# Performance work log

Hardware: AMD Instinct MI355X
Metric: run time of the kernel (lower is better)

## Reference

```python
import jax, jax.numpy as jnp
import numpy as np

WIDTH_POW = 10
WIDTH = 2 ** WIDTH_POW          # 1024
HALF = WIDTH // 2               # 512
DEPTH = 8                       # number of butterfly layers
BDEPTH = 10                     # steps per butterfly (= log2(width))
BATCH = 65536
NUM_IN = WIDTH
NUM_OUT = WIDTH


def setup_inputs() -> dict:
    key = jax.random.key(0)
    k1, k2, k3, k4, k5 = jax.random.split(key, 5)
    X = jax.random.normal(k1, (BATCH, NUM_IN), dtype=jnp.float32)
    # rotation angles uniform in [0, 2*pi): (depth, half_width, bdepth)
    bparams = jax.random.uniform(k2, (DEPTH, HALF, BDEPTH), dtype=jnp.float32) * (2.0 * np.pi)
    eps = 1.0 / WIDTH
    n_act = DEPTH - 1
    bias = jax.random.uniform(k3, (n_act, WIDTH), dtype=jnp.float32) * (2 * eps) - eps
    slope = jax.random.uniform(k4, (n_act, WIDTH), dtype=jnp.float32) * (2 * eps) - eps + 1.0
    scale = jax.random.uniform(k5, (n_act, WIDTH), dtype=jnp.float32) * (2 * eps) - eps + 1.0
    return {"X": X, "bparams": bparams, "bias": bias, "slope": slope, "scale": scale}


def _butterfly(X, params):
    """params: (half, bdepth). One OrthogonalButterfly layer."""
    def step(X, theta):
        c = jnp.cos(theta)          # (half,)
        s = jnp.sin(theta)
        X0 = X[:, :HALF]
        X1 = X[:, HALF:]
        n0 = X0 * c + X1 * s
        n1 = -X0 * s + X1 * c
        # perm: even i -> n0[i//2], odd i -> n1[i//2]  == interleave n0, n1
        Xn = jnp.stack([n0, n1], axis=-1).reshape(X.shape[0], WIDTH)
        return Xn, None
    X, _ = jax.lax.scan(step, X, params.T)  # iterate over bdepth
    return X


def _quintic(X, bias, slope, scale):
    u = jnp.clip((X * slope - bias) / scale, -1.0, 1.0)
    u2 = u * u
    return scale * (u * (1.875 + u2 * (-1.25 + 0.375 * u2)))


def reference(X, bparams, bias, slope, scale):
    # num_inputs == width, so the zero-padding concat is a no-op.
    for i in range(DEPTH):
        X = _butterfly(X, bparams[i])
        if i != DEPTH - 1:
            X = _quintic(X, bias[i], slope[i], scale[i])
    return X[:, :NUM_OUT]
```

## Files before the change

kernel.cpp:

```cpp
#include <hip/hip_runtime.h>
#include <hip/hip_bf16.h>

#define WIDTH   1024
#define HALF_W  512
#define DEPTH   8
#define BDEPTH  10
#define BATCH   65536
#define ROWS    16
#define S_R     32
#define S_H     520

typedef _Float16 v8h __attribute__((ext_vector_type(8)));
typedef float    v4f __attribute__((ext_vector_type(4)));

static __device__ __forceinline__ unsigned short f2h(float x) {
    _Float16 h = (_Float16)x;
    return __builtin_bit_cast(unsigned short, h);
}

__global__ void gen_mats(const float* __restrict__ bp, unsigned short* __restrict__ mats)
{
    const int bid = blockIdx.x;
    const int grp = bid & 31;
    const int ph  = (bid >> 5) & 1;
    const int L   = bid >> 6;
    const int tid = threadIdx.x;

    __shared__ float M[2][32][32];

    for (int i = tid; i < 1024; i += 64)
        M[0][i >> 5][i & 31] = ((i >> 5) == (i & 31)) ? 1.0f : 0.0f;
    __syncthreads();

    int buf = 0;
    for (int s = 0; s < 5; ++s) {
        const int t = ph * 5 + s;
        const int stride = 1 << (4 - s);
        for (int idx = tid; idx < 512; idx += 64) {
            const int a  = idx >> 5;
            const int c  = idx & 31;
            const int lo = ((a & ~(stride - 1)) << 1) | (a & (stride - 1));
            const int hi = lo | stride;
            const int p_low = (ph == 0) ? ((lo << 5) | grp) : ((grp << 5) | lo);
            const int j = (((p_low << t) | (p_low >> (10 - t))) & 1023) & 511;
            const float theta = bp[L * (HALF_W * BDEPTH) + j * BDEPTH + t];
            float sn, cs;
            sincosf(theta, &sn, &cs);
            const float xl = M[buf][lo][c];
            const float xh = M[buf][hi][c];
            M[1 - buf][lo][c] =  cs * xl + sn * xh;
            M[1 - buf][hi][c] = -sn * xl + cs * xh;
        }
        buf = 1 - buf;
        __syncthreads();
    }

    unsigned short* out = mats + (size_t)bid * 1024;
    for (int i = tid; i < 1024; i += 64) {
        const int nt   = i >> 9;
        const int lane = (i >> 3) & 63;
        const int jj   = i & 7;
        const int n = nt * 16 + (lane & 15);
        const int k = (lane >> 4) * 8 + jj;
        out[i] = f2h(M[buf][n][k]);
    }
}

__global__ void __launch_bounds__(256, 2) butterfly_net(
    const float* __restrict__ X,
    const unsigned short* __restrict__ mats,
    const float* __restrict__ bias,
    const float* __restrict__ slope,
    const float* __restrict__ scale,
    float* __restrict__ out)
{
    __shared__ unsigned short X1[32 * S_H];
    __shared__ unsigned short X2[32 * S_H];

    const int tid  = threadIdx.x;
    const int lane = tid & 63;
    const int w    = tid >> 6;
    const int lw   = lane & 15;
    const int q    = lane >> 4;
    const int row0 = blockIdx.x * ROWS;

    for (int it = 0; it < 16; ++it) {
        const int f = (it * 256 + tid) * 4;
        const int r = f >> 10;
        const int c = f & 1023;
        const float4 v = *(const float4*)(X + (size_t)(row0 + r) * WIDTH + c);
        const int h  = c >> 5;
        const int g0 = c & 31;
        X1[(g0 + 0) * S_H + r * S_R + h] = f2h(v.x);
        X1[(g0 + 1) * S_H + r * S_R + h] = f2h(v.y);
        X1[(g0 + 2) * S_H + r * S_R + h] = f2h(v.z);
        X1[(g0 + 3) * S_H + r * S_R + h] = f2h(v.w);
    }
    __syncthreads();

    for (int L = 0; L < DEPTH; ++L) {
        const unsigned short* m1 = mats + (size_t)(L * 2 + 0) * 32 * 1024;
        for (int s = 0; s < 2; ++s) {
            const int gbase = w * 8 + s * 4;
            v4f C[4][2];
            #pragma unroll
            for (int gi = 0; gi < 4; ++gi) {
                const int g = gbase + gi;
                const v8h A = *(const v8h*)&X1[g * S_H + lw * S_R + q * 8];
                #pragma unroll
                for (int nt = 0; nt < 2; ++nt) {
                    const v8h B = *(const v8h*)&m1[(size_t)g * 1024 + nt * 512 + lane * 8];
                    C[gi][nt] = __builtin_amdgcn_mfma_f32_16x16x32_f16(
                        A, B, (v4f){0.0f, 0.0f, 0.0f, 0.0f}, 0, 0, 0);
                }
            }
            #pragma unroll
            for (int nt = 0; nt < 2; ++nt) {
                const int hout = nt * 16 + lw;
                #pragma unroll
                for (int r = 0; r < 4; ++r) {
                    const int row = q * 4 + r;
                    ushort4 pk;
                    pk.x = f2h(C[0][nt][r]);
                    pk.y = f2h(C[1][nt][r]);
                    pk.z = f2h(C[2][nt][r]);
                    pk.w = f2h(C[3][nt][r]);
                    *(ushort4*)&X2[hout * S_H + row * S_R + gbase] = pk;
                }
            }
        }
        __syncthreads();

        const unsigned short* m2 = mats + (size_t)(L * 2 + 1) * 32 * 1024;
        const bool last = (L == DEPTH - 1);
        for (int s = 0; s < 2; ++s) {
            const int hbase = w * 8 + s * 4;
            v4f C[4][2];
            #pragma unroll
            for (int hi2 = 0; hi2 < 4; ++hi2) {
                const int h = hbase + hi2;
                const v8h A = *(const v8h*)&X2[h * S_H + lw * S_R + q * 8];
                #pragma unroll
                for (int nt = 0; nt < 2; ++nt) {
                    const v8h B = *(const v8h*)&m2[(size_t)h * 1024 + nt * 512 + lane * 8];
                    C[hi2][nt] = __builtin_amdgcn_mfma_f32_16x16x32_f16(
                        A, B, (v4f){0.0f, 0.0f, 0.0f, 0.0f}, 0, 0, 0);
                }
            }
            if (!last) {
                #pragma unroll
                for (int nt = 0; nt < 2; ++nt) {
                    const int gout = nt * 16 + lw;
                    float bia[4], slo[4], sca[4], rsc[4];
                    #pragma unroll
                    for (int hi2 = 0; hi2 < 4; ++hi2) {
                        const int p = (hbase + hi2) * 32 + gout;
                        bia[hi2] = bias [L * WIDTH + p];
                        slo[hi2] = slope[L * WIDTH + p];
                        sca[hi2] = scale[L * WIDTH + p];
                        rsc[hi2] = 1.0f / sca[hi2];
                    }
                    #pragma unroll
                    for (int r = 0; r < 4; ++r) {
                        const int row = q * 4 + r;
                        ushort4 pk;
                        unsigned short* pp = (unsigned short*)&pk;
                        #pragma unroll
                        for (int hi2 = 0; hi2 < 4; ++hi2) {
                            const float x = C[hi2][nt][r];
                            float u = (x * slo[hi2] - bia[hi2]) * rsc[hi2];
                            u = fminf(1.0f, fmaxf(-1.0f, u));
                            const float u2 = u * u;
                            const float y = sca[hi2] *
                                (u * (1.875f + u2 * (-1.25f + 0.375f * u2)));
                            pp[hi2] = f2h(y);
                        }
                        *(ushort4*)&X1[gout * S_H + row * S_R + hbase] = pk;
                    }
                }
            } else {
                #pragma unroll
                for (int nt = 0; nt < 2; ++nt) {
                    const int gout = nt * 16 + lw;
                    #pragma unroll
                    for (int hi2 = 0; hi2 < 4; ++hi2) {
                        const int h = hbase + hi2;
                        #pragma unroll
                        for (int r = 0; r < 4; ++r) {
                            const int row = q * 4 + r;
                            out[(size_t)(row0 + row) * WIDTH + h * 32 + gout] =
                                C[hi2][nt][r];
                        }
                    }
                }
            }
        }
        __syncthreads();
    }
}

extern "C" void kernel_launch(void* const* d_in, const int* in_sizes, int n_in,
                              void* d_out, int out_size, void* d_ws, size_t ws_size,
                              hipStream_t stream)
{
    const float* X     = (const float*)d_in[0];
    const float* bp    = (const float*)d_in[1];
    const float* bias  = (const float*)d_in[2];
    const float* slope = (const float*)d_in[3];
    const float* scale = (const float*)d_in[4];
    unsigned short* mats = (unsigned short*)d_ws;

    hipLaunchKernelGGL(gen_mats, dim3(512), dim3(64), 0, stream, bp, mats);
    hipLaunchKernelGGL(butterfly_net, dim3(BATCH / ROWS), dim3(256), 0, stream,
                       X, mats, bias, slope, scale, (float*)d_out);
}
```

Before: 708.4 us.

## Use single in-place swizzled LDS buffer, 32-row blocks, and precomputed activation params

Replaces the two padded LDS buffers with one XOR-swizzled 64KB buffer. A-fragments are loaded into registers and a barrier is taken before the results are written back in place. Blocks grow to 512 threads handling 32 rows, so each loaded B matrix fragment is reused across two row groups. A small pre-kernel folds bias, slope and scale into packed float4 coefficients, removing divides and separate loads from the activation. The input load is restructured to do strided reads per thread. The main risks are an extra barrier per stage and lower occupancy from the larger block and LDS footprint.

Result: slower. 1.110 ms (+56.6%).

```diff
diff --git a/kernel.cpp b/kernel.cpp
--- a/kernel.cpp
+++ b/kernel.cpp
@@ -1,21 +1,24 @@
 #include <hip/hip_runtime.h>
-#include <hip/hip_bf16.h>
 
 #define WIDTH   1024
 #define HALF_W  512
 #define DEPTH   8
 #define BDEPTH  10
 #define BATCH   65536
-#define ROWS    16
-#define S_R     32
-#define S_H     520
+#define ROWS    32
 
 typedef _Float16 v8h __attribute__((ext_vector_type(8)));
+typedef _Float16 v4h __attribute__((ext_vector_type(4)));
 typedef float    v4f __attribute__((ext_vector_type(4)));
 
 static __device__ __forceinline__ unsigned short f2h(float x) {
     _Float16 h = (_Float16)x;
     return __builtin_bit_cast(unsigned short, h);
+}
+
+static __device__ __forceinline__ int xoff(int slice, int r, int k) {
+    int b = (slice << 11) + (r << 6) + (k << 1);
+    return b ^ ((((r >> 1) ^ slice) & 7) << 4);
 }
 
 __global__ void gen_mats(const float* __restrict__ bp, unsigned short* __restrict__ mats)
@@ -66,136 +69,143 @@
     }
 }
 
-__global__ void __launch_bounds__(256, 2) butterfly_net(
+__global__ void fuse_act(const float* __restrict__ bias,
+                         const float* __restrict__ slope,
+                         const float* __restrict__ scale,
+                         float4* __restrict__ actT)
+{
+    const int i = blockIdx.x * 256 + threadIdx.x;
+    if (i < (DEPTH - 1) * WIDTH) {
+        const float b = bias[i], s = slope[i], c = scale[i];
+        const float r = 1.0f / c;
+        actT[i] = make_float4(s * r, b * r, c, 0.0f);
+    }
+}
+
+__global__ void __launch_bounds__(512, 4) butterfly_net(
     const float* __restrict__ X,
     const unsigned short* __restrict__ mats,
-    const float* __restrict__ bias,
-    const float* __restrict__ slope,
-    const float* __restrict__ scale,
+    const float4* __restrict__ actT,
     float* __restrict__ out)
 {
-    __shared__ unsigned short X1[32 * S_H];
-    __shared__ unsigned short X2[32 * S_H];
+    __shared__ unsigned char Xb[32 * 2048];
 
     const int tid  = threadIdx.x;
     const int lane = tid & 63;
-    const int w    = tid >> 6;
+    const int wv   = tid >> 6;
+    const int oct  = wv & 3;
+    const int rg   = wv >> 2;
     const int lw   = lane & 15;
     const int q    = lane >> 4;
     const int row0 = blockIdx.x * ROWS;
-
-    for (int it = 0; it < 16; ++it) {
-        const int f = (it * 256 + tid) * 4;
-        const int r = f >> 10;
-        const int c = f & 1023;
-        const float4 v = *(const float4*)(X + (size_t)(row0 + r) * WIDTH + c);
-        const int h  = c >> 5;
-        const int g0 = c & 31;
-        X1[(g0 + 0) * S_H + r * S_R + h] = f2h(v.x);
-        X1[(g0 + 1) * S_H + r * S_R + h] = f2h(v.y);
-        X1[(g0 + 2) * S_H + r * S_R + h] = f2h(v.z);
-        X1[(g0 + 3) * S_H + r * S_R + h] = f2h(v.w);
+    const int rbase = rg * 16;
+
+    {
+        const int g = tid & 31;
+        const int m = tid >> 5;
+        #pragma unroll
+        for (int it = 0; it < 8; ++it) {
+            const int cmb = it * 16 + m;
+            const int r   = cmb >> 2;
+            const int h0  = (cmb & 3) * 8;
+            const float* src = X + (size_t)(row0 + r) * WIDTH + (size_t)h0 * 32 + g;
+            v8h pk;
+            #pragma unroll
+            for (int j = 0; j < 8; ++j)
+                pk[j] = (_Float16)src[j * 32];
+            *(v8h*)(Xb + xoff(g, r, h0)) = pk;
+        }
     }
     __syncthreads();
 
     for (int L = 0; L < DEPTH; ++L) {
-        const unsigned short* m1 = mats + (size_t)(L * 2 + 0) * 32 * 1024;
-        for (int s = 0; s < 2; ++s) {
-            const int gbase = w * 8 + s * 4;
-            v4f C[4][2];
-            #pragma unroll
-            for (int gi = 0; gi < 4; ++gi) {
-                const int g = gbase + gi;
-                const v8h A = *(const v8h*)&X1[g * S_H + lw * S_R + q * 8];
+        const bool last = (L == DEPTH - 1);
+
+        {
+            const unsigned short* m1 = mats + (size_t)(L * 2 + 0) * 32 * 1024;
+            v8h aF[8];
+            #pragma unroll
+            for (int i = 0; i < 8; ++i)
+                aF[i] = *(const v8h*)(Xb + xoff(oct * 8 + i, rbase + lw, q * 8));
+            __syncthreads();
+            #pragma unroll
+            for (int s = 0; s < 2; ++s) {
+                const int gbase = oct * 8 + s * 4;
                 #pragma unroll
                 for (int nt = 0; nt < 2; ++nt) {
-                    const v8h B = *(const v8h*)&m1[(size_t)g * 1024 + nt * 512 + lane * 8];
-                    C[gi][nt] = __builtin_amdgcn_mfma_f32_16x16x32_f16(
-                        A, B, (v4f){0.0f, 0.0f, 0.0f, 0.0f}, 0, 0, 0);
+                    v4f C[4];
+                    #pragma unroll
+                    for (int gi = 0; gi < 4; ++gi) {
+                        const v8h B = *(const v8h*)&m1[(size_t)(gbase + gi) * 1024
+                                                       + nt * 512 + lane * 8];
+                        C[gi] = __builtin_amdgcn_mfma_f32_16x16x32_f16(
+                            aF[s * 4 + gi], B, (v4f){0.f, 0.f, 0.f, 0.f}, 0, 0, 0);
+                    }
+                    const int hout = nt * 16 + lw;
+                    #pragma unroll
+                    for (int r = 0; r < 4; ++r) {
+                        v4h pk = { (_Float16)C[0][r], (_Float16)C[1][r],
+                                   (_Float16)C[2][r], (_Float16)C[3][r] };
+                        *(v4h*)(Xb + xoff(hout, rbase + q * 4 + r, gbase)) = pk;
+                    }
                 }
             }
-            #pragma unroll
-            for (int nt = 0; nt < 2; ++nt) {
-                const int hout = nt * 16 + lw;
+            __syncthreads();
+        }
+
+        {
+            const unsigned short* m2 = mats + (size_t)(L * 2 + 1) * 32 * 1024;
+            v8h aF[8];
+            #pragma unroll
+            for (int i = 0; i < 8; ++i)
+                aF[i] = *(const v8h*)(Xb + xoff(oct * 8 + i, rbase + lw, q * 8));
+            __syncthreads();
+            #pragma unroll
+            for (int s = 0; s < 2; ++s) {
+                const int hbase = oct * 8 + s * 4;
                 #pragma unroll
-                for (int r = 0; r < 4; ++r) {
-                    const int row = q * 4 + r;
-                    ushort4 pk;
-                    pk.x = f2h(C[0][nt][r]);
-                    pk.y = f2h(C[1][nt][r]);
-                    pk.z = f2h(C[2][nt][r]);
-                    pk.w = f2h(C[3][nt][r]);
-                    *(ushort4*)&X2[hout * S_H + row * S_R + gbase] = pk;
+                for (int nt = 0; nt < 2; ++nt) {
+                    v4f C[4];
+                    #pragma unroll
+                    for (int hi = 0; hi < 4; ++hi) {
+                        const v8h B = *(const v8h*)&m2[(size_t)(hbase + hi) * 1024
+                                                       + nt * 512 + lane * 8];
+                        C[hi] = __builtin_amdgcn_mfma_f32_16x16x32_f16(
+                            aF[s * 4 + hi], B, (v4f){0.f, 0.f, 0.f, 0.f}, 0, 0, 0);
+                    }
+                    const int gout = nt * 16 + lw;
+                    if (!last) {
+                        float4 ac[4];
+                        #pragma unroll
+                        for (int hi = 0; hi < 4; ++hi)
+                            ac[hi] = actT[(size_t)L * WIDTH + (hbase + hi) * 32 + gout];
+                        #pragma unroll
+                        for (int r = 0; r < 4; ++r) {
+                            v4h pk;
+                            #pragma unroll
+                            for (int hi = 0; hi < 4; ++hi) {
+                                float u = fmaf(C[hi][r], ac[hi].x, -ac[hi].y);
+                                u = fminf(1.0f, fmaxf(-1.0f, u));
+                                const float u2 = u * u;
+                                const float p5 = fmaf(u2, 0.375f, -1.25f);
+                                const float p3 = fmaf(u2, p5, 1.875f);
+                                pk[hi] = (_Float16)(u * p3 * ac[hi].z);
+                            }
+                            *(v4h*)(Xb + xoff(gout, rbase + q * 4 + r, hbase)) = pk;
+                        }
+                    } else {
+                        #pragma unroll
+                        for (int hi = 0; hi < 4; ++hi) {
+                            #pragma unroll
+                            for (int r = 0; r < 4; ++r)
+                                out[(size_t)(row0 + rbase + q * 4 + r) * WIDTH
+                                    + (hbase + hi) * 32 + gout] = C[hi][r];
+                        }
+                    }
                 }
             }
-        }
-        __syncthreads();
-
-        const unsigned short* m2 = mats + (size_t)(L * 2 + 1) * 32 * 1024;
-        const bool last = (L == DEPTH - 1);
-        for (int s = 0; s < 2; ++s) {
-            const int hbase = w * 8 + s * 4;
-            v4f C[4][2];
-            #pragma unroll
-            for (int hi2 = 0; hi2 < 4; ++hi2) {
-                const int h = hbase + hi2;
-                const v8h A = *(const v8h*)&X2[h * S_H + lw * S_R + q * 8];
-                #pragma unroll
-                for (int nt = 0; nt < 2; ++nt) {
-                    const v8h B = *(const v8h*)&m2[(size_t)h * 1024 + nt * 512 + lane * 8];
-                    C[hi2][nt] = __builtin_amdgcn_mfma_f32_16x16x32_f16(
-                        A, B, (v4f){0.0f, 0.0f, 0.0f, 0.0f}, 0, 0, 0);
-                }
-            }
-            if (!last) {
-                #pragma unroll
-                for (int nt = 0; nt < 2; ++nt) {
-                    const int gout = nt * 16 + lw;
-                    float bia[4], slo[4], sca[4], rsc[4];
-                    #pragma unroll
-                    for (int hi2 = 0; hi2 < 4; ++hi2) {
-                        const int p = (hbase + hi2) * 32 + gout;
-                        bia[hi2] = bias [L * WIDTH + p];
-                        slo[hi2] = slope[L * WIDTH + p];
-                        sca[hi2] = scale[L * WIDTH + p];
-                        rsc[hi2] = 1.0f / sca[hi2];
-                    }
-                    #pragma unroll
-                    for (int r = 0; r < 4; ++r) {
-                        const int row = q * 4 + r;
-                        ushort4 pk;
-                        unsigned short* pp = (unsigned short*)&pk;
-                        #pragma unroll
-                        for (int hi2 = 0; hi2 < 4; ++hi2) {
-                            const float x = C[hi2][nt][r];
-                            float u = (x * slo[hi2] - bia[hi2]) * rsc[hi2];
-                            u = fminf(1.0f, fmaxf(-1.0f, u));
-                            const float u2 = u * u;
-                            const float y = sca[hi2] *
-                                (u * (1.875f + u2 * (-1.25f + 0.375f * u2)));
-                            pp[hi2] = f2h(y);
-                        }
-                        *(ushort4*)&X1[gout * S_H + row * S_R + hbase] = pk;
-                    }
-                }
-            } else {
-                #pragma unroll
-                for (int nt = 0; nt < 2; ++nt) {
-                    const int gout = nt * 16 + lw;
-                    #pragma unroll
-                    for (int hi2 = 0; hi2 < 4; ++hi2) {
-                        const int h = hbase + hi2;
-                        #pragma unroll
-                        for (int r = 0; r < 4; ++r) {
-                            const int row = q * 4 + r;
-                            out[(size_t)(row0 + row) * WIDTH + h * 32 + gout] =
-                                C[hi2][nt][r];
-                        }
-                    }
-                }
-            }
-        }
-        __syncthreads();
+            if (!last) __syncthreads();
+        }
     }
 }
 
@@ -209,8 +219,11 @@
     const float* slope = (const float*)d_in[3];
     const float* scale = (const float*)d_in[4];
     unsigned short* mats = (unsigned short*)d_ws;
+    float4* actT = (float4*)((char*)d_ws + 512 * 1024 * 2);
 
     hipLaunchKernelGGL(gen_mats, dim3(512), dim3(64), 0, stream, bp, mats);
-    hipLaunchKernelGGL(butterfly_net, dim3(BATCH / ROWS), dim3(256), 0, stream,
-                       X, mats, bias, slope, scale, (float*)d_out);
-}
+    hipLaunchKernelGGL(fuse_act, dim3(((DEPTH - 1) * WIDTH + 255) / 256), dim3(256),
+                       0, stream, bias, slope, scale, actT);
+    hipLaunchKernelGGL(butterfly_net, dim3(BATCH / ROWS), dim3(512), 0, stream,
+                       X, mats, actT, (float*)d_out);
+}
```
